# Kernel tuning notes

Hardware: AMD Instinct MI355X
Metric: run time of the kernel (lower is better)

Reference implementation:

```python
import jax, jax.numpy as jnp
import numpy as np

EMB = 128
EDGE = 32
STEPS = 3


def _lrelu(x):
    return jax.nn.leaky_relu(x, negative_slope=0.01)


def setup_inputs() -> dict:
    key = jax.random.key(0)
    ks = jax.random.split(key, 16)
    N, E, G = 50000, 400000, 256
    x = jax.random.normal(ks[0], (N, EMB), jnp.float32)
    edge_attr = jax.random.normal(ks[1], (E, EDGE), jnp.float32)
    edge_index = jax.random.randint(ks[2], (2, E), 0, N, jnp.int64)
    batch_ind = jnp.sort(jax.random.randint(ks[3], (N,), 0, G, jnp.int64))
    data_lens = jax.random.randint(ks[4], (G,), 0, G, jnp.int64)
    s = 1.0 / np.sqrt(EMB)
    Wm = jax.random.normal(ks[5], (STEPS, EMB + EDGE, EMB), jnp.float32) * s
    bm = jnp.zeros((STEPS, EMB), jnp.float32)
    Wa = jax.random.normal(ks[6], (STEPS, 3 * EMB, EMB), jnp.float32) * s
    ba = jnp.zeros((STEPS, EMB), jnp.float32)
    Wgate = jax.random.normal(ks[7], (STEPS, EMB), jnp.float32) * s
    bgate = jnp.zeros((STEPS,), jnp.float32)
    Wfeat = jax.random.normal(ks[8], (STEPS, EMB, EMB), jnp.float32) * s
    bfeat = jnp.zeros((STEPS, EMB), jnp.float32)
    Wt = jax.random.normal(ks[9], (STEPS, 2 * EMB, EMB), jnp.float32) * s
    bt = jnp.zeros((STEPS, EMB), jnp.float32)
    return {"x": x, "edge_attr": edge_attr, "Wm": Wm, "bm": bm, "Wa": Wa,
            "ba": ba, "Wgate": Wgate, "bgate": bgate, "Wfeat": Wfeat,
            "bfeat": bfeat, "Wt": Wt, "bt": bt, "edge_index": edge_index,
            "batch_ind": batch_ind, "num_graphs": 256, "data_lens": data_lens}


def reference(x, edge_attr, Wm, bm, Wa, ba, Wgate, bgate, Wfeat, bfeat, Wt, bt,
              edge_index, batch_ind, num_graphs, data_lens):
    N = x.shape[0]
    src, dst = edge_index[0], edge_index[1]  # PyG: x_j = x[src], aggregate at dst
    xg = jnp.zeros((num_graphs, EMB), x.dtype)  # xg_init is None -> zeros
    for s in range(STEPS):
        # GraphNet: gather -> message MLP -> scatter-max -> update MLP + residual
        xg_node = xg[batch_ind]                                   # [N, emb]
        z = jnp.concatenate([x[src], edge_attr], axis=1)          # [E, emb+edge]
        m = _lrelu(z @ Wm[s] + bm[s])                             # [E, emb]
        agg = jax.ops.segment_max(m, dst, num_segments=N)         # [N, emb]
        agg = jnp.where(jnp.isneginf(agg), 0.0, agg)              # PyG fills empty with 0
        z2 = jnp.concatenate([x, xg_node, agg], axis=1)           # [N, 3*emb]
        x = _lrelu(z2 @ Wa[s] + ba[s]) + x
        # GlobalNode: segment-softmax attention pooling + transform + residual
        gate = x @ Wgate[s] + bgate[s]                            # [N]
        gmax = jax.ops.segment_max(gate, batch_ind, num_segments=num_graphs)
        gmax = jnp.where(jnp.isneginf(gmax), 0.0, gmax)
        e = jnp.exp(gate - gmax[batch_ind])
        denom = jax.ops.segment_sum(e, batch_ind, num_segments=num_graphs)
        alpha = e / denom[batch_ind]                              # [N]
        feat = _lrelu(x @ Wfeat[s] + bfeat[s])                    # [N, emb]
        pooled = jax.ops.segment_sum(alpha[:, None] * feat, batch_ind,
                                     num_segments=num_graphs)     # [G, emb]
        cat = jnp.concatenate([pooled, xg], axis=1)               # [G, 2*emb]
        xg = _lrelu(cat @ Wt[s] + bt[s]) + xg
    return x, xg
```

## Files before the change

### kernel.cpp

```cpp
#include <hip/hip_runtime.h>
#include <hip/hip_bf16.h>

#define EMB 128
#define EDGE 32
#define STEPS 3

typedef short bf8s __attribute__((ext_vector_type(8)));
typedef float f32x4 __attribute__((ext_vector_type(4)));
typedef unsigned short u16x4 __attribute__((ext_vector_type(4)));

__device__ __forceinline__ float lrelu(float v) { return v > 0.0f ? v : 0.01f * v; }
__device__ __forceinline__ unsigned short f2bf(float f) {
    unsigned u = __float_as_uint(f);
    u += 0x7fffu + ((u >> 16) & 1u);
    return (unsigned short)(u >> 16);
}
__device__ __forceinline__ float bf2f(unsigned short s) {
    return __uint_as_float(((unsigned)s) << 16);
}
__device__ __forceinline__ unsigned pk2bf(float x, float y) {
    __hip_bfloat162 h = __float22bfloat162_rn(make_float2(x, y));
    return *(unsigned*)&h;
}

__global__ void k_hist(const int* __restrict__ dst, int E, int* __restrict__ deg) {
    int e = blockIdx.x * 256 + threadIdx.x;
    if (e < E) atomicAdd(&deg[dst[e]], 1);
}

__global__ void k_scan1(const int* __restrict__ deg, int N, int* __restrict__ rowptr,
                        int* __restrict__ bsums) {
    __shared__ int s[256];
    int t = threadIdx.x;
    int i = blockIdx.x * 256 + t;
    int v = (i < N) ? deg[i] : 0;
    s[t] = v;
    __syncthreads();
#pragma unroll
    for (int off = 1; off < 256; off <<= 1) {
        int x = (t >= off) ? s[t - off] : 0;
        __syncthreads();
        s[t] += x;
        __syncthreads();
    }
    if (i < N) rowptr[i] = s[t] - v;
    if (t == 255) bsums[blockIdx.x] = s[255];
}

__global__ void k_scan2(int* __restrict__ bsums, int NB) {
    __shared__ int s[256];
    __shared__ int carry;
    int t = threadIdx.x;
    if (t == 0) carry = 0;
    __syncthreads();
    for (int base = 0; base < NB; base += 256) {
        int i = base + t;
        int v = (i < NB) ? bsums[i] : 0;
        s[t] = v;
        __syncthreads();
#pragma unroll
        for (int off = 1; off < 256; off <<= 1) {
            int x = (t >= off) ? s[t - off] : 0;
            __syncthreads();
            s[t] += x;
            __syncthreads();
        }
        int excl = s[t] - v + carry;
        if (i < NB) bsums[i] = excl;
        int tot = s[255];
        __syncthreads();
        if (t == 0) carry += tot;
        __syncthreads();
    }
}

__global__ void k_scan3(int* __restrict__ rowptr, const int* __restrict__ bsums, int N, int E) {
    int i = blockIdx.x * 256 + threadIdx.x;
    if (i < N) rowptr[i] += bsums[i >> 8];
    if (i == 0) rowptr[N] = E;
}

__global__ void k_fill(const int* __restrict__ src, const int* __restrict__ dst, int E,
                       int* __restrict__ cursor, int2* __restrict__ slot) {
    int e = blockIdx.x * 256 + threadIdx.x;
    if (e < E) {
        int d = dst[e];
        int p = atomicAdd(&cursor[d], 1);
        slot[p] = make_int2(src[e], e);
    }
}

__global__ void k_gstart(const int* __restrict__ batch, int N, int G, int* __restrict__ gstart) {
    int g = blockIdx.x * blockDim.x + threadIdx.x;
    if (g > G) return;
    int lo = 0, hi = N;
    while (lo < hi) {
        int mid = (lo + hi) >> 1;
        if (batch[mid] < g) lo = mid + 1; else hi = mid;
    }
    gstart[g] = lo;
}

__global__ __launch_bounds__(256) void k_wpack(const float* __restrict__ Wm,
                                               const float* __restrict__ Wa,
                                               const float* __restrict__ Wfeat,
                                               unsigned short* __restrict__ wpack) {
    int gid = blockIdx.x * 256 + threadIdx.x;
    int unit = gid >> 14;
    int e = gid & 16383;
    int s = unit / 5, u = unit % 5;
    const float* src; int rows;
    switch (u) {
        case 0: src = Wm + (size_t)s * 160 * EMB;             rows = 128; break;
        case 1: src = Wm + (size_t)s * 160 * EMB + 128 * EMB; rows = 32;  break;
        case 2: src = Wa + (size_t)s * 384 * EMB;             rows = 128; break;
        case 3: src = Wa + (size_t)s * 384 * EMB + 256 * EMB; rows = 128; break;
        default: src = Wfeat + (size_t)s * EMB * EMB;         rows = 128; break;
    }
    int k = e >> 7, n = e & 127;
    if (k >= rows) return;
    unsigned short b = f2bf(src[(size_t)k * EMB + n]);
    int kc = k >> 5, c = n >> 4, lane = (n & 15) | (((k & 31) >> 3) << 4), j = k & 7;
    wpack[(size_t)unit * 16384 + ((size_t)(kc * 8 + c) * 64 + lane) * 8 + j] = b;
}

__device__ __forceinline__ void loadAx(const float* __restrict__ A, int row0, int wv,
                                       int lane, int N, bf8s af[4]) {
    int li = lane & 15, oct = lane >> 4;
    int m = row0 + wv * 16 + li;
    if (m >= N) m = N - 1;
    const float4* xr = (const float4*)(A + (size_t)m * EMB);
#pragma unroll
    for (int kc = 0; kc < 4; ++kc) {
        float4 a0 = xr[kc * 8 + oct * 2];
        float4 a1 = xr[kc * 8 + oct * 2 + 1];
        union { bf8s v; unsigned u[4]; } c;
        c.u[0] = pk2bf(a0.x, a0.y);
        c.u[1] = pk2bf(a0.z, a0.w);
        c.u[2] = pk2bf(a1.x, a1.y);
        c.u[3] = pk2bf(a1.z, a1.w);
        af[kc] = c.v;
    }
}
__device__ __forceinline__ void loadAa(const unsigned short* __restrict__ A16, int row0,
                                       int wv, int lane, int N, bf8s af[4]) {
    int li = lane & 15, oct = lane >> 4;
    int m = row0 + wv * 16 + li;
    if (m >= N) m = N - 1;
    const bf8s* ar = (const bf8s*)(A16 + (size_t)m * EMB);
#pragma unroll
    for (int kc = 0; kc < 4; ++kc) af[kc] = ar[kc * 4 + oct];
}
__device__ __forceinline__ void stageB(const unsigned short* __restrict__ Bp,
                                       unsigned short* lB, int tid) {
#pragma unroll
    for (int i = 0; i < 8; ++i) {
        int idx = tid + i * 256;
        ((int4*)lB)[idx] = ((const int4*)Bp)[idx];
    }
}
__device__ __forceinline__ void mfma128r(const bf8s af[4], const unsigned short* lB,
                                         f32x4 acc[8], int lane) {
#pragma unroll
    for (int kc = 0; kc < 4; ++kc) {
#pragma unroll
        for (int c = 0; c < 8; ++c) {
            bf8s b = *(const bf8s*)&lB[((kc * 8 + c) * 64 + lane) * 8];
            acc[c] = __builtin_amdgcn_mfma_f32_16x16x32_bf16(af[kc], b, acc[c], 0, 0, 0);
        }
    }
}

__global__ __launch_bounds__(256) void k_gemm_bias(const float* __restrict__ A,
                                                   const unsigned short* __restrict__ Bp,
                                                   const float* __restrict__ bias,
                                                   unsigned short* __restrict__ C, int N) {
    __shared__ unsigned short lB[16384];
    int tid = threadIdx.x, wv = tid >> 6, lane = tid & 63;
    int row0 = blockIdx.x * 64;
    stageB(Bp, lB, tid);
    bf8s af[4];
    loadAx(A, row0, wv, lane, N, af);
    __syncthreads();
    f32x4 acc[8];
#pragma unroll
    for (int c = 0; c < 8; ++c) acc[c] = (f32x4){0.f, 0.f, 0.f, 0.f};
    mfma128r(af, lB, acc, lane);
    int li = lane & 15, quad = lane >> 4;
    float bcol[8];
#pragma unroll
    for (int c = 0; c < 8; ++c) bcol[c] = bias[c * 16 + li];
#pragma unroll
    for (int rr = 0; rr < 4; ++rr) {
        int m = row0 + wv * 16 + quad * 4 + rr;
        if (m < N) {
            union { bf8s v; unsigned u[4]; } o;
#pragma unroll
            for (int j = 0; j < 4; ++j)
                o.u[j] = pk2bf(acc[2 * j][rr] + bcol[2 * j],
                               acc[2 * j + 1][rr] + bcol[2 * j + 1]);
            *(bf8s*)&C[(size_t)m * EMB + li * 8] = o.v;
        }
    }
}

__global__ __launch_bounds__(256) void k_gemm_node(const float* __restrict__ x,
                                                   const unsigned short* __restrict__ agg16,
                                                   const unsigned short* __restrict__ BpX,
                                                   const unsigned short* __restrict__ BpA,
                                                   const float* __restrict__ gb,
                                                   const int* __restrict__ batch,
                                                   float* __restrict__ xout,
                                                   const float* __restrict__ wg,
                                                   const float* __restrict__ bg,
                                                   float* __restrict__ gate, int N) {
    __shared__ unsigned short lB[16384];
    int tid = threadIdx.x, wv = tid >> 6, lane = tid & 63;
    int row0 = blockIdx.x * 64;
    stageB(BpX, lB, tid);
    bf8s af[4];
    loadAx(x, row0, wv, lane, N, af);
    __syncthreads();
    f32x4 acc[8];
#pragma unroll
    for (int c = 0; c < 8; ++c) acc[c] = (f32x4){0.f, 0.f, 0.f, 0.f};
    mfma128r(af, lB, acc, lane);
    __syncthreads();
    stageB(BpA, lB, tid);
    loadAa(agg16, row0, wv, lane, N, af);
    __syncthreads();
    mfma128r(af, lB, acc, lane);
    int li = lane & 15, quad = lane >> 4;
    float gpart[4] = {0.f, 0.f, 0.f, 0.f};
#pragma unroll
    for (int c = 0; c < 8; ++c) {
        int col = c * 16 + li;
        float wgc = wg[col];
#pragma unroll
        for (int rr = 0; rr < 4; ++rr) {
            int m = row0 + wv * 16 + quad * 4 + rr;
            if (m < N) {
                int g = batch[m];
                float b = gb[(size_t)g * EMB + col];
                float res = x[(size_t)m * EMB + col];
                float v = lrelu(acc[c][rr] + b) + res;
                xout[(size_t)m * EMB + col] = v;
                gpart[rr] = fmaf(v, wgc, gpart[rr]);
            }
        }
    }
#pragma unroll
    for (int rr = 0; rr < 4; ++rr) {
#pragma unroll
        for (int off = 1; off < 16; off <<= 1)
            gpart[rr] += __shfl_xor(gpart[rr], off, 64);
    }
    if (li == 0) {
        float b0 = bg[0];
#pragma unroll
        for (int rr = 0; rr < 4; ++rr) {
            int m = row0 + wv * 16 + quad * 4 + rr;
            if (m < N) gate[m] = gpart[rr] + b0;
        }
    }
}

__global__ __launch_bounds__(256) void k_gemm_feat(const float* __restrict__ A,
                                                   const unsigned short* __restrict__ Bp,
                                                   const float* __restrict__ bias,
                                                   const float* __restrict__ gate,
                                                   const float* __restrict__ gmax,
                                                   const float* __restrict__ denom,
                                                   const int* __restrict__ batch,
                                                   unsigned short* __restrict__ C, int N) {
    __shared__ unsigned short lB[16384];
    int tid = threadIdx.x, wv = tid >> 6, lane = tid & 63;
    int row0 = blockIdx.x * 64;
    stageB(Bp, lB, tid);
    bf8s af[4];
    loadAx(A, row0, wv, lane, N, af);
    __syncthreads();
    f32x4 acc[8];
#pragma unroll
    for (int c = 0; c < 8; ++c) acc[c] = (f32x4){0.f, 0.f, 0.f, 0.f};
    mfma128r(af, lB, acc, lane);
    int li = lane & 15, quad = lane >> 4;
    float alpha[4];
#pragma unroll
    for (int rr = 0; rr < 4; ++rr) {
        int m = row0 + wv * 16 + quad * 4 + rr;
        if (m < N) {
            int g = batch[m];
            alpha[rr] = __expf(gate[m] - gmax[g]) / denom[g];
        } else alpha[rr] = 0.f;
    }
#pragma unroll
    for (int c = 0; c < 8; ++c) {
        int col = c * 16 + li;
        float b = bias[col];
#pragma unroll
        for (int rr = 0; rr < 4; ++rr) {
            int m = row0 + wv * 16 + quad * 4 + rr;
            if (m < N) C[(size_t)m * EMB + col] = f2bf(alpha[rr] * lrelu(acc[c][rr] + b));
        }
    }
}

__global__ __launch_bounds__(256) void k_fagg(const unsigned short* __restrict__ h,
                                              const float* __restrict__ ea,
                                              const int2* __restrict__ slot,
                                              const int* __restrict__ rowptr,
                                              const unsigned short* __restrict__ Bp,
                                              unsigned short* __restrict__ agg, int N) {
    __shared__ unsigned short lB[4096];
    int tid = threadIdx.x;
    ((int4*)lB)[tid]       = ((const int4*)Bp)[tid];
    ((int4*)lB)[tid + 256] = ((const int4*)Bp)[tid + 256];
    __syncthreads();
    int wv = tid >> 6, lane = tid & 63;
    int n = blockIdx.x * 4 + wv;
    if (n >= N) return;
    int li = lane & 15, oct = lane >> 4;
    int r0 = rowptr[n], r1 = rowptr[n + 1], deg = r1 - r0;

    float vm[8];
#pragma unroll
    for (int ci = 0; ci < 8; ++ci) vm[ci] = -__builtin_inff();

    for (int b = 0; b < deg; b += 16) {
        int p = r0 + b + li;
        if (p > r1 - 1) p = r1 - 1;
        int2 sl = slot[p];
        const float4* ear = (const float4*)(ea + (size_t)sl.y * EDGE);
        float4 v0 = ear[oct * 2], v1 = ear[oct * 2 + 1];
        union { bf8s v; unsigned u[4]; } ac;
        ac.u[0] = pk2bf(v0.x, v0.y);
        ac.u[1] = pk2bf(v0.z, v0.w);
        ac.u[2] = pk2bf(v1.x, v1.y);
        ac.u[3] = pk2bf(v1.z, v1.w);
        bf8s a = ac.v;
        bool val_r[4];
        union { bf8s v; unsigned short s[8]; } hv[4];
#pragma unroll
        for (int rr = 0; rr < 4; ++rr) {
            int src = __shfl(sl.x, oct * 4 + rr, 16);
            val_r[rr] = (b + oct * 4 + rr) < deg;
            hv[rr].v = *(const bf8s*)&h[(size_t)src * EMB + li * 8];
        }
#pragma unroll
        for (int ci = 0; ci < 8; ++ci) {
            bf8s bb = *(const bf8s*)&lB[(ci * 64 + lane) * 8];
            f32x4 acc;
            acc[0] = bf2f(hv[0].s[ci]);
            acc[1] = bf2f(hv[1].s[ci]);
            acc[2] = bf2f(hv[2].s[ci]);
            acc[3] = bf2f(hv[3].s[ci]);
            acc = __builtin_amdgcn_mfma_f32_16x16x32_bf16(a, bb, acc, 0, 0, 0);
#pragma unroll
            for (int rr = 0; rr < 4; ++rr)
                if (val_r[rr]) vm[ci] = fmaxf(vm[ci], acc[rr]);
        }
    }
#pragma unroll
    for (int ci = 0; ci < 8; ++ci) {
        vm[ci] = fmaxf(vm[ci], __shfl_xor(vm[ci], 16, 64));
        vm[ci] = fmaxf(vm[ci], __shfl_xor(vm[ci], 32, 64));
    }
    float s0 = (oct == 0) ? vm[0] : (oct == 1) ? vm[1] : (oct == 2) ? vm[2] : vm[3];
    float s1 = (oct == 0) ? vm[4] : (oct == 1) ? vm[5] : (oct == 2) ? vm[6] : vm[7];
    s0 = lrelu(s0);
    s1 = lrelu(s1);
    if (deg == 0) { s0 = 0.f; s1 = 0.f; }
    agg[(size_t)n * EMB + oct * 16 + li]        = f2bf(s0);
    agg[(size_t)n * EMB + (oct + 4) * 16 + li]  = f2bf(s1);
}

__global__ __launch_bounds__(128) void k_gb(const float* __restrict__ xg,
                                            const float* __restrict__ WaG,
                                            const float* __restrict__ ba,
                                            float* __restrict__ gb) {
    int g = blockIdx.x, c = threadIdx.x;
    __shared__ float row[EMB];
    row[c] = xg[(size_t)g * EMB + c];
    __syncthreads();
    float acc = ba[c];
#pragma unroll 8
    for (int k = 0; k < EMB; ++k) acc = fmaf(row[k], WaG[(size_t)k * EMB + c], acc);
    gb[(size_t)g * EMB + c] = acc;
}

__global__ __launch_bounds__(256) void k_gseg(const float* __restrict__ gate,
                                              const int* __restrict__ gstart,
                                              float* __restrict__ gmax,
                                              float* __restrict__ denom) {
    int g = blockIdx.x;
    int s0 = gstart[g], s1 = gstart[g + 1];
    __shared__ float red[256];
    int t = threadIdx.x;
    float mx = -__builtin_inff();
    for (int i = s0 + t; i < s1; i += 256) mx = fmaxf(mx, gate[i]);
    red[t] = mx;
    __syncthreads();
#pragma unroll
    for (int off = 128; off; off >>= 1) {
        if (t < off) red[t] = fmaxf(red[t], red[t + off]);
        __syncthreads();
    }
    float m = red[0];
    __syncthreads();
    float sum = 0.f;
    for (int i = s0 + t; i < s1; i += 256) sum += __expf(gate[i] - m);
    red[t] = sum;
    __syncthreads();
#pragma unroll
    for (int off = 128; off; off >>= 1) {
        if (t < off) red[t] += red[t + off];
        __syncthreads();
    }
    if (t == 0) {
        gmax[g] = (s1 > s0) ? m : 0.f;
        denom[g] = red[0];
    }
}

__global__ __launch_bounds__(512) void k_pool(const unsigned short* __restrict__ feat,
                                              const int* __restrict__ gstart,
                                              float* __restrict__ pooled) {
    int g = blockIdx.x;
    int c = threadIdx.x & 127;
    int r = threadIdx.x >> 7;
    int s0 = gstart[g], s1 = gstart[g + 1];
    float s = 0.f;
    for (int i = s0 + r; i < s1; i += 4) s += bf2f(feat[(size_t)i * EMB + c]);
    __shared__ float red[512];
    red[threadIdx.x] = s;
    __syncthreads();
    if (threadIdx.x < 256) red[threadIdx.x] += red[threadIdx.x + 256];
    __syncthreads();
    if (threadIdx.x < 128)
        pooled[(size_t)g * EMB + threadIdx.x] = red[threadIdx.x] + red[threadIdx.x + 128];
}

__global__ __launch_bounds__(128) void k_xg(const float* __restrict__ pooled,
                                            const float* __restrict__ xg,
                                            const float* __restrict__ Wt,
                                            const float* __restrict__ bt,
                                            float* __restrict__ xg_out) {
    int g = blockIdx.x, c = threadIdx.x;
    __shared__ float row[256];
    row[c] = pooled[(size_t)g * EMB + c];
    row[c + 128] = xg[(size_t)g * EMB + c];
    __syncthreads();
    float acc = bt[c];
#pragma unroll 8
    for (int k = 0; k < 256; ++k) acc = fmaf(row[k], Wt[(size_t)k * EMB + c], acc);
    xg_out[(size_t)g * EMB + c] = lrelu(acc) + row[c + 128];
}

extern "C" void kernel_launch(void* const* d_in, const int* in_sizes, int n_in,
                              void* d_out, int out_size, void* d_ws, size_t ws_size,
                              hipStream_t stream) {
    const float* x0    = (const float*)d_in[0];
    const float* ea    = (const float*)d_in[1];
    const float* Wm    = (const float*)d_in[2];
    const float* bm    = (const float*)d_in[3];
    const float* Wa    = (const float*)d_in[4];
    const float* ba    = (const float*)d_in[5];
    const float* Wgate = (const float*)d_in[6];
    const float* bgate = (const float*)d_in[7];
    const float* Wfeat = (const float*)d_in[8];
    const float* bfeat = (const float*)d_in[9];
    const float* Wt    = (const float*)d_in[10];
    const float* bt    = (const float*)d_in[11];
    const int*   eidx  = (const int*)d_in[12];
    const int*   batch = (const int*)d_in[13];

    int N = in_sizes[0] / EMB;
    int E = in_sizes[1] / EDGE;
    int G = in_sizes[15];

    char* w = (char*)d_ws;
    auto alloc = [&](size_t bytes) {
        char* p = w;
        w += (bytes + 255) & ~(size_t)255;
        return p;
    };
    unsigned short* h16   = (unsigned short*)alloc((size_t)N * EMB * 2);
    unsigned short* agg16 = (unsigned short*)alloc((size_t)N * EMB * 2);
    unsigned short* ft16  = (unsigned short*)alloc((size_t)N * EMB * 2);
    float* gate   = (float*)alloc((size_t)N * 4);
    float* gb     = (float*)alloc((size_t)G * EMB * 4);
    float* pooled = (float*)alloc((size_t)G * EMB * 4);
    float* gmax   = (float*)alloc((size_t)G * 4);
    float* denom  = (float*)alloc((size_t)G * 4);
    float* xg_a   = (float*)alloc((size_t)G * EMB * 4);
    float* xg_b   = (float*)alloc((size_t)G * EMB * 4);
    int* deg      = (int*)alloc((size_t)N * 4);
    int* rowptr   = (int*)alloc((size_t)(N + 1) * 4);
    int* cursor   = (int*)alloc((size_t)N * 4);
    int2* slot    = (int2*)alloc((size_t)E * 8);
    int* gstart   = (int*)alloc((size_t)(G + 1) * 4);
    int* bsums    = (int*)alloc(1024 * 4);
    unsigned short* wpack = (unsigned short*)alloc((size_t)15 * 16384 * 2);

    const int* esrc = eidx;
    const int* edst = eidx + E;
    int ebl = (E + 255) / 256;
    int NB  = (N + 255) / 256;

    hipMemsetAsync(deg, 0, (size_t)N * 4, stream);
    k_hist<<<ebl, 256, 0, stream>>>(edst, E, deg);
    k_scan1<<<NB, 256, 0, stream>>>(deg, N, rowptr, bsums);
    k_scan2<<<1, 256, 0, stream>>>(bsums, NB);
    k_scan3<<<NB, 256, 0, stream>>>(rowptr, bsums, N, E);
    hipMemcpyAsync(cursor, rowptr, (size_t)N * 4, hipMemcpyDeviceToDevice, stream);
    k_fill<<<ebl, 256, 0, stream>>>(esrc, edst, E, cursor, slot);
    k_gstart<<<(G + 256) / 256, 256, 0, stream>>>(batch, N, G, gstart);
    hipMemsetAsync(xg_a, 0, (size_t)G * EMB * 4, stream);
    k_wpack<<<960, 256, 0, stream>>>(Wm, Wa, Wfeat, wpack);

    int gemm_blocks = (N + 63) / 64;
    int fagg_blocks = (N + 3) / 4;

    const float* x_in = x0;
    float* xg_cur = xg_a;
    float* xg_nxt = xg_b;

    for (int s = 0; s < STEPS; ++s) {
        const unsigned short* wp = wpack + (size_t)s * 5 * 16384;
        float* x_out = (s == STEPS - 1) ? (float*)d_out : (float*)x_in;

        k_gemm_bias<<<gemm_blocks, 256, 0, stream>>>(x_in, wp + 0 * 16384, bm + s * EMB,
                                                     h16, N);
        k_fagg<<<fagg_blocks, 256, 0, stream>>>(h16, ea, slot, rowptr, wp + 1 * 16384,
                                                agg16, N);
        k_gb<<<G, 128, 0, stream>>>(xg_cur, Wa + (size_t)s * 384 * EMB + 128 * EMB,
                                    ba + s * EMB, gb);
        k_gemm_node<<<gemm_blocks, 256, 0, stream>>>(x_in, agg16, wp + 2 * 16384,
                                                     wp + 3 * 16384, gb, batch, x_out,
                                                     Wgate + s * EMB, bgate + s, gate, N);
        k_gseg<<<G, 256, 0, stream>>>(gate, gstart, gmax, denom);
        k_gemm_feat<<<gemm_blocks, 256, 0, stream>>>(x_out, wp + 4 * 16384, bfeat + s * EMB,
                                                     gate, gmax, denom, batch, ft16, N);
        k_pool<<<G, 512, 0, stream>>>(ft16, gstart, pooled);
        k_xg<<<G, 128, 0, stream>>>(pooled, xg_cur, Wt + (size_t)s * 256 * EMB,
                                    bt + s * EMB, xg_nxt);

        x_in = x_out;
        float* tmp = xg_cur; xg_cur = xg_nxt; xg_nxt = tmp;
    }

    hipMemcpyAsync((float*)d_out + (size_t)N * EMB, xg_cur, (size_t)G * EMB * 4,
                   hipMemcpyDeviceToDevice, stream);
}
```

Baseline: 620.9 us.

## Pre-permute edge attributes to bf16 in CSR order and use a sentinel row for padding

```diff
diff --git a/kernel.cpp b/kernel.cpp
--- a/kernel.cpp
+++ b/kernel.cpp
@@ -7,7 +7,6 @@
 
 typedef short bf8s __attribute__((ext_vector_type(8)));
 typedef float f32x4 __attribute__((ext_vector_type(4)));
-typedef unsigned short u16x4 __attribute__((ext_vector_type(4)));
 
 __device__ __forceinline__ float lrelu(float v) { return v > 0.0f ? v : 0.01f * v; }
 __device__ __forceinline__ unsigned short f2bf(float f) {
@@ -80,14 +79,30 @@
     if (i == 0) rowptr[N] = E;
 }
 
-__global__ void k_fill(const int* __restrict__ src, const int* __restrict__ dst, int E,
-                       int* __restrict__ cursor, int2* __restrict__ slot) {
+__global__ void k_fill(const int* __restrict__ src, const int* __restrict__ dst,
+                       const float* __restrict__ ea, int E,
+                       int* __restrict__ cursor, int* __restrict__ srcp,
+                       unsigned short* __restrict__ ea16p) {
     int e = blockIdx.x * 256 + threadIdx.x;
-    if (e < E) {
-        int d = dst[e];
-        int p = atomicAdd(&cursor[d], 1);
-        slot[p] = make_int2(src[e], e);
-    }
+    if (e >= E) return;
+    int d = dst[e];
+    int p = atomicAdd(&cursor[d], 1);
+    srcp[p] = src[e];
+    const float4* er = (const float4*)(ea + (size_t)e * EDGE);
+    union { unsigned u[16]; int4 v[4]; } o;
+#pragma unroll
+    for (int q = 0; q < 8; ++q) {
+        float4 v = er[q];
+        o.u[2 * q]     = pk2bf(v.x, v.y);
+        o.u[2 * q + 1] = pk2bf(v.z, v.w);
+    }
+    int4* dp = (int4*)(ea16p + (size_t)p * EDGE);
+#pragma unroll
+    for (int q = 0; q < 4; ++q) dp[q] = o.v[q];
+}
+
+__global__ void k_hsent(unsigned short* __restrict__ h, int N) {
+    h[(size_t)N * EMB + threadIdx.x] = 0xFF80u;
 }
 
 __global__ void k_gstart(const int* __restrict__ batch, int N, int G, int* __restrict__ gstart) {
@@ -307,8 +322,8 @@
 }
 
 __global__ __launch_bounds__(256) void k_fagg(const unsigned short* __restrict__ h,
-                                              const float* __restrict__ ea,
-                                              const int2* __restrict__ slot,
+                                              const unsigned short* __restrict__ ea16p,
+                                              const int* __restrict__ srcp,
                                               const int* __restrict__ rowptr,
                                               const unsigned short* __restrict__ Bp,
                                               unsigned short* __restrict__ agg, int N) {
@@ -330,22 +345,14 @@
     for (int b = 0; b < deg; b += 16) {
         int p = r0 + b + li;
         if (p > r1 - 1) p = r1 - 1;
-        int2 sl = slot[p];
-        const float4* ear = (const float4*)(ea + (size_t)sl.y * EDGE);
-        float4 v0 = ear[oct * 2], v1 = ear[oct * 2 + 1];
-        union { bf8s v; unsigned u[4]; } ac;
-        ac.u[0] = pk2bf(v0.x, v0.y);
-        ac.u[1] = pk2bf(v0.z, v0.w);
-        ac.u[2] = pk2bf(v1.x, v1.y);
-        ac.u[3] = pk2bf(v1.z, v1.w);
-        bf8s a = ac.v;
-        bool val_r[4];
+        int srcv = srcp[p];
+        bf8s a = *(const bf8s*)&ea16p[(size_t)p * EDGE + oct * 8];
         union { bf8s v; unsigned short s[8]; } hv[4];
 #pragma unroll
         for (int rr = 0; rr < 4; ++rr) {
-            int src = __shfl(sl.x, oct * 4 + rr, 16);
-            val_r[rr] = (b + oct * 4 + rr) < deg;
-            hv[rr].v = *(const bf8s*)&h[(size_t)src * EMB + li * 8];
+            int sr = __shfl(srcv, oct * 4 + rr, 16);
+            if (b + oct * 4 + rr >= deg) sr = N;
+            hv[rr].v = *(const bf8s*)&h[(size_t)sr * EMB + li * 8];
         }
 #pragma unroll
         for (int ci = 0; ci < 8; ++ci) {
@@ -357,8 +364,7 @@
             acc[3] = bf2f(hv[3].s[ci]);
             acc = __builtin_amdgcn_mfma_f32_16x16x32_bf16(a, bb, acc, 0, 0, 0);
 #pragma unroll
-            for (int rr = 0; rr < 4; ++rr)
-                if (val_r[rr]) vm[ci] = fmaxf(vm[ci], acc[rr]);
+            for (int rr = 0; rr < 4; ++rr) vm[ci] = fmaxf(vm[ci], acc[rr]);
         }
     }
 #pragma unroll
@@ -485,7 +491,7 @@
         w += (bytes + 255) & ~(size_t)255;
         return p;
     };
-    unsigned short* h16   = (unsigned short*)alloc((size_t)N * EMB * 2);
+    unsigned short* h16   = (unsigned short*)alloc((size_t)(N + 1) * EMB * 2);
     unsigned short* agg16 = (unsigned short*)alloc((size_t)N * EMB * 2);
     unsigned short* ft16  = (unsigned short*)alloc((size_t)N * EMB * 2);
     float* gate   = (float*)alloc((size_t)N * 4);
@@ -498,7 +504,8 @@
     int* deg      = (int*)alloc((size_t)N * 4);
     int* rowptr   = (int*)alloc((size_t)(N + 1) * 4);
     int* cursor   = (int*)alloc((size_t)N * 4);
-    int2* slot    = (int2*)alloc((size_t)E * 8);
+    int* srcp     = (int*)alloc((size_t)E * 4);
+    unsigned short* ea16p = (unsigned short*)alloc((size_t)E * EDGE * 2);
     int* gstart   = (int*)alloc((size_t)(G + 1) * 4);
     int* bsums    = (int*)alloc(1024 * 4);
     unsigned short* wpack = (unsigned short*)alloc((size_t)15 * 16384 * 2);
@@ -514,7 +521,8 @@
     k_scan2<<<1, 256, 0, stream>>>(bsums, NB);
     k_scan3<<<NB, 256, 0, stream>>>(rowptr, bsums, N, E);
     hipMemcpyAsync(cursor, rowptr, (size_t)N * 4, hipMemcpyDeviceToDevice, stream);
-    k_fill<<<ebl, 256, 0, stream>>>(esrc, edst, E, cursor, slot);
+    k_fill<<<ebl, 256, 0, stream>>>(esrc, edst, ea, E, cursor, srcp, ea16p);
+    k_hsent<<<1, 128, 0, stream>>>(h16, N);
     k_gstart<<<(G + 256) / 256, 256, 0, stream>>>(batch, N, G, gstart);
     hipMemsetAsync(xg_a, 0, (size_t)G * EMB * 4, stream);
     k_wpack<<<960, 256, 0, stream>>>(Wm, Wa, Wfeat, wpack);
@@ -532,7 +540,7 @@
 
         k_gemm_bias<<<gemm_blocks, 256, 0, stream>>>(x_in, wp + 0 * 16384, bm + s * EMB,
                                                      h16, N);
-        k_fagg<<<fagg_blocks, 256, 0, stream>>>(h16, ea, slot, rowptr, wp + 1 * 16384,
+        k_fagg<<<fagg_blocks, 256, 0, stream>>>(h16, ea16p, srcp, rowptr, wp + 1 * 16384,
                                                 agg16, N);
         k_gb<<<G, 128, 0, stream>>>(xg_cur, Wa + (size_t)s * 384 * EMB + 128 * EMB,
                                     ba + s * EMB, gb);
```

Result: faster. 596.8 us (-3.9%).
